# Kernel optimization log

Measured on AMD Instinct MI355X. Metric: run time of the kernel, lower is better.

Reference implementation:

```python
import jax, jax.numpy as jnp
import numpy as np

ROPE_BASE = 10000.0

def apply_rope(x, offset=0):
    # x: [B, H, L, Dh], traditional (interleaved-pair) RoPE
    B, H, L, Dh = x.shape
    pos = jnp.arange(L, dtype=jnp.float32) + offset            # [L]
    freqs = ROPE_BASE ** (-jnp.arange(0, Dh, 2, dtype=jnp.float32) / Dh)  # [Dh/2]
    theta = pos[:, None] * freqs[None, :]                      # [L, Dh/2]
    cos, sin = jnp.cos(theta), jnp.sin(theta)
    x1 = x[..., 0::2]                                          # [B,H,L,Dh/2]
    x2 = x[..., 1::2]
    r1 = x1 * cos - x2 * sin
    r2 = x1 * sin + x2 * cos
    return jnp.stack([r1, r2], axis=-1).reshape(B, H, L, Dh)


def setup_inputs() -> dict:
    key = jax.random.key(0)
    ks = jax.random.split(key, 5)
    B, L, D = 2, 2048, 2048
    s = 1.0 / np.sqrt(D)
    x = jax.random.normal(ks[0], (B, L, D), dtype=jnp.float32)
    # additive causal mask (0 on/below diagonal, -1e9 above)
    mask = jnp.where(jnp.tril(jnp.ones((L, L), dtype=bool)), 0.0, -1e9).astype(jnp.float32)
    Wq = jax.random.normal(ks[1], (D, D), dtype=jnp.float32) * s
    Wk = jax.random.normal(ks[2], (D, D), dtype=jnp.float32) * s
    Wv = jax.random.normal(ks[3], (D, D), dtype=jnp.float32) * s
    Wo = jax.random.normal(ks[4], (D, D), dtype=jnp.float32) * s
    return {"x": x, "mask": mask, "Wq": Wq, "Wk": Wk, "Wv": Wv, "Wo": Wo}


def reference(x, mask, Wq, Wk, Wv, Wo):
    num_heads = 16
    B, L, D = x.shape
    Dh = D // num_heads
    q = (x @ Wq.T).reshape(B, L, num_heads, Dh).transpose(0, 2, 1, 3)  # [B,H,L,Dh]
    k = (x @ Wk.T).reshape(B, L, num_heads, Dh).transpose(0, 2, 1, 3)
    v = (x @ Wv.T).reshape(B, L, num_heads, Dh).transpose(0, 2, 1, 3)
    q = apply_rope(q)
    k = apply_rope(k)
    scale = 1.0 / jnp.sqrt(jnp.float32(Dh))
    scores = jnp.einsum('bhqd,bhkd->bhqk', q * scale, k) + mask  # [B,H,L,L]
    probs = jax.nn.softmax(scores, axis=-1)
    vh = jnp.einsum('bhqk,bhkd->bhqd', probs, v)                 # [B,H,L,Dh]
    vh = vh.transpose(0, 2, 1, 3).reshape(B, L, D)
    out = vh @ Wo.T
    return out, k, v
```

## Files before the change

### kernel.cpp

```cpp
#include <hip/hip_runtime.h>

typedef __attribute__((ext_vector_type(4))) float f32x4;
typedef __attribute__((ext_vector_type(8))) __bf16 bf16x8;

__device__ __forceinline__ unsigned short f2b(float f) {
  unsigned int u = __builtin_bit_cast(unsigned int, f);
  u = (u + 0x7fffu + ((u >> 16) & 1u)) >> 16;
  return (unsigned short)u;
}
__device__ __forceinline__ float b2f(unsigned short h) {
  unsigned int u = ((unsigned int)h) << 16;
  return __builtin_bit_cast(float, u);
}
__device__ __forceinline__ void gl_lds16(const void* g, void* l) {
  __builtin_amdgcn_global_load_lds(
      (const __attribute__((address_space(1))) void*)g,
      (__attribute__((address_space(3))) void*)l, 16, 0, 0);
}

__global__ void cast_kernel(const float* __restrict__ src,
                            unsigned short* __restrict__ dst, int n4) {
  int i = blockIdx.x * blockDim.x + threadIdx.x;
  if (i >= n4) return;
  float4 v = ((const float4*)src)[i];
  ushort4 o;
  o.x = f2b(v.x); o.y = f2b(v.y); o.z = f2b(v.z); o.w = f2b(v.w);
  ((ushort4*)dst)[i] = o;
}

__global__ void cast4_kernel(const float* __restrict__ s0, const float* __restrict__ s1,
                             const float* __restrict__ s2, const float* __restrict__ s3,
                             unsigned short* __restrict__ d0, unsigned short* __restrict__ d1,
                             unsigned short* __restrict__ d2, unsigned short* __restrict__ d3,
                             int n4) {
  int i = blockIdx.x * blockDim.x + threadIdx.x;
  if (i >= n4) return;
  const float* src = blockIdx.y == 0 ? s0 : blockIdx.y == 1 ? s1 : blockIdx.y == 2 ? s2 : s3;
  unsigned short* dst = blockIdx.y == 0 ? d0 : blockIdx.y == 1 ? d1 : blockIdx.y == 2 ? d2 : d3;
  float4 v = ((const float4*)src)[i];
  ushort4 o;
  o.x = f2b(v.x); o.y = f2b(v.y); o.z = f2b(v.z); o.w = f2b(v.w);
  ((ushort4*)dst)[i] = o;
}

__global__ void rope_table_kernel(float2* __restrict__ tab) {
  int idx = blockIdx.x * blockDim.x + threadIdx.x;
  int l = idx >> 6, i = idx & 63;
  float freq = powf(10000.0f, -(float)(2 * i) / 128.0f);
  float th = (float)l * freq;
  tab[idx] = make_float2(cosf(th), sinf(th));
}

__global__ void rope_apply_kernel(unsigned short* __restrict__ qb,
                                  unsigned short* __restrict__ kb,
                                  unsigned short* __restrict__ vb,
                                  float* __restrict__ kout,
                                  float* __restrict__ vout,
                                  const float2* __restrict__ tab) {
  const float QS = 0.12751743f;
  int z = blockIdx.y;
  int p = blockIdx.x * blockDim.x + threadIdx.x;
  int i = p & 63;
  int t = p >> 6;
  int h = t & 15; t >>= 4;
  int l = t & 2047;
  int b = t >> 11;
  int base = ((b * 2048 + l) * 2048) + h * 128 + 2 * i;
  int obase = ((b * 16 + h) * 2048 + l) * 128 + 2 * i;
  if (z == 2) {
    vout[obase] = b2f(vb[base]);
    vout[obase + 1] = b2f(vb[base + 1]);
  } else {
    unsigned short* buf = z ? kb : qb;
    float x1 = b2f(buf[base]), x2 = b2f(buf[base + 1]);
    float2 cs = tab[l * 64 + i];
    float r1 = x1 * cs.x - x2 * cs.y;
    float r2 = x1 * cs.y + x2 * cs.x;
    if (z == 1) {
      buf[base] = f2b(r1);
      buf[base + 1] = f2b(r2);
      kout[obase] = r1; kout[obase + 1] = r2;
    } else {
      buf[base] = f2b(r1 * QS);
      buf[base + 1] = f2b(r2 * QS);
    }
  }
}

__global__ __launch_bounds__(256) void transpose_v_kernel(const unsigned short* __restrict__ vb,
                                                          unsigned short* __restrict__ vt) {
  __shared__ unsigned short t[32][33];
  int bz = blockIdx.z;
  int b = bz >> 4, h = bz & 15;
  int l0 = blockIdx.x * 32, d0 = blockIdx.y * 32;
  const unsigned short* src = vb + (size_t)b * 2048 * 2048 + h * 128;
  unsigned short* dst = vt + (size_t)bz * 128 * 2048;
  int tx = threadIdx.x & 31, ty = threadIdx.x >> 5;
#pragma unroll
  for (int i = 0; i < 4; ++i)
    t[ty + 8 * i][tx] = src[(size_t)(l0 + ty + 8 * i) * 2048 + d0 + tx];
  __syncthreads();
#pragma unroll
  for (int i = 0; i < 4; ++i)
    dst[(size_t)(d0 + ty + 8 * i) * 2048 + l0 + tx] = t[tx][ty + 8 * i];
}

template <int BM, int NBN, int OUT_F32>
__global__ __launch_bounds__(512, 2) void gemm4(const unsigned short* __restrict__ A,
                                                const unsigned short* __restrict__ W,
                                                void* __restrict__ C) {
  constexpr int K = 2048, NT = 32;
  constexpr int AH = BM / 2;
  constexpr int MF = BM / 64;
  constexpr int AQ = AH / 64;
  __shared__ unsigned short Asm[2][2][AH * 64];
  __shared__ unsigned short Bsm[2][2][128 * 64];

  const int tid = threadIdx.x, lane = tid & 63, wv = tid >> 6;
  const int wr = wv >> 2, wc = wv & 3;
  const int ln = lane & 15, kg = lane >> 4;

  const int cpx = (int)gridDim.x >> 3;
  const int swzb = ((int)blockIdx.x & 7) * cpx + ((int)blockIdx.x >> 3);
  const int bm = swzb / NBN, bn = swzb % NBN;
  const int m0 = bm * BM, n0 = bn * 256;

  const int rr = lane >> 3;
  const int sws = ((lane & 7) ^ (rr & 7)) * 8;
  const unsigned short* pA = A + (size_t)(m0 + wv * 8 * AQ + rr) * K + sws;
  const unsigned short* pB = W + (size_t)(n0 + wv * 16 + rr) * K + sws;

#define STA_(dd, hh, tt)                                                         \
  { _Pragma("unroll") for (int q = 0; q < AQ; ++q)                               \
      gl_lds16(pA + ((size_t)(hh)*AH + q * 8) * K + (size_t)(tt)*64,             \
               &Asm[dd][hh][(wv * 8 * AQ + q * 8) * 64 + lane * 8]); }
#define STB_(dd, hh, tt)                                                         \
  { _Pragma("unroll") for (int q = 0; q < 2; ++q)                                \
      gl_lds16(pB + ((size_t)(hh)*128 + q * 8) * K + (size_t)(tt)*64,            \
               &Bsm[dd][hh][(wv * 16 + q * 8) * 64 + lane * 8]); }

  const int sw0 = (kg ^ (ln & 7)) * 8;
  const int sw1 = ((4 + kg) ^ (ln & 7)) * 8;
  const int rae = (wr * (AH / 2) + ln) * 64;
  const int rbe = (wc * 32 + ln) * 64;

  f32x4 acc[2 * MF][4] = {};
  bf16x8 aA[MF][2], bB[2][2][2];

#define LDA_(dd, mh)                                                              \
  { _Pragma("unroll") for (int mf = 0; mf < MF; ++mf) {                           \
      aA[mf][0] = *(const bf16x8*)&Asm[dd][mh][rae + mf * 1024 + sw0];            \
      aA[mf][1] = *(const bf16x8*)&Asm[dd][mh][rae + mf * 1024 + sw1];            \
    } }
#define LDB_(dd, bh)                                                              \
  { _Pragma("unroll") for (int nf = 0; nf < 2; ++nf) {                            \
      bB[bh][nf][0] = *(const bf16x8*)&Bsm[dd][bh][rbe + nf * 1024 + sw0];        \
      bB[bh][nf][1] = *(const bf16x8*)&Bsm[dd][bh][rbe + nf * 1024 + sw1];        \
    } }

#define QMM(mh, bh)                                                               \
  {                                                                               \
    __builtin_amdgcn_s_setprio(1);                                                \
    _Pragma("unroll") for (int mf = 0; mf < MF; ++mf)                             \
        _Pragma("unroll") for (int nf = 0; nf < 2; ++nf) {                        \
      acc[(mh)*MF + mf][(bh)*2 + nf] = __builtin_amdgcn_mfma_f32_16x16x32_bf16(   \
          aA[mf][0], bB[bh][nf][0], acc[(mh)*MF + mf][(bh)*2 + nf], 0, 0, 0);     \
      acc[(mh)*MF + mf][(bh)*2 + nf] = __builtin_amdgcn_mfma_f32_16x16x32_bf16(   \
          aA[mf][1], bB[bh][nf][1], acc[(mh)*MF + mf][(bh)*2 + nf], 0, 0, 0);     \
    }                                                                             \
    __builtin_amdgcn_s_setprio(0);                                                \
  }

#define BAR   { __builtin_amdgcn_s_barrier(); __builtin_amdgcn_sched_barrier(0); }
#define VWAIT                                                                     \
  { if (BM == 256) { asm volatile("s_waitcnt vmcnt(4)" ::: "memory"); }           \
    else { asm volatile("s_waitcnt vmcnt(3)" ::: "memory"); } }
#define VW0   { asm volatile("s_waitcnt vmcnt(0)" ::: "memory"); }

  STA_(0, 0, 0); STB_(0, 0, 0); STB_(0, 1, 0); STA_(0, 1, 0);
  STA_(1, 0, 1); STB_(1, 1, 1);
  VWAIT;

  for (int T = 0; T < NT; T += 2) {
    const bool more = (T + 2) < NT;
    LDA_(0, 0); LDB_(0, 0);
    STB_(1, 0, T + 1);
    BAR; QMM(0, 0); BAR;
    LDB_(0, 1);
    STA_(1, 1, T + 1);
    BAR; QMM(0, 1); BAR;
    LDA_(0, 1);
    if (more) STA_(0, 0, T + 2);
    BAR; QMM(1, 1); BAR;
    if (more) { STB_(0, 1, T + 2); VWAIT; } else { VW0; }
    BAR; QMM(1, 0); BAR;
    LDA_(1, 0); LDB_(1, 0);
    if (more) STB_(0, 0, T + 2);
    BAR; QMM(0, 0); BAR;
    LDB_(1, 1);
    if (more) STA_(0, 1, T + 2);
    BAR; QMM(0, 1); BAR;
    LDA_(1, 1);
    if (more) STA_(1, 0, T + 3);
    BAR; QMM(1, 1); BAR;
    if (more) { STB_(1, 1, T + 3); VWAIT; }
    BAR; QMM(1, 0); BAR;
  }

  const int mat = bn >> 3;
  unsigned short* Cb = (unsigned short*)C;
  float* Cf = (float*)C;
#pragma unroll
  for (int mh = 0; mh < 2; ++mh)
#pragma unroll
    for (int mf = 0; mf < MF; ++mf)
#pragma unroll
      for (int j = 0; j < 4; ++j) {
        int row = m0 + mh * AH + wr * (AH / 2) + mf * 16 + kg * 4 + j;
        size_t rb = (size_t)mat * 8388608 + (size_t)row * 2048 + (size_t)((bn & 7) * 256);
#pragma unroll
        for (int bh = 0; bh < 2; ++bh)
#pragma unroll
          for (int nf = 0; nf < 2; ++nf) {
            int col = bh * 128 + wc * 32 + nf * 16 + ln;
            float v = acc[mh * MF + mf][bh * 2 + nf][j];
            if (OUT_F32) Cf[rb + col] = v;
            else Cb[rb + col] = f2b(v);
          }
      }
#undef STA_
#undef STB_
#undef LDA_
#undef LDB_
#undef QMM
#undef BAR
#undef VWAIT
#undef VW0
}

__global__ __launch_bounds__(256, 2) void attn3_kernel(const unsigned short* __restrict__ Qb,
                                                       const unsigned short* __restrict__ Kb,
                                                       const unsigned short* __restrict__ Vt,
                                                       unsigned short* __restrict__ Ob) {
  __shared__ unsigned short KS[2][8192];
  __shared__ unsigned short VS[2][8192];
  __shared__ unsigned short PS[4][2048];
  const int D = 2048, L = 2048;
  int tid = threadIdx.x, lane = tid & 63, w = tid >> 6;
  int ln = lane & 15, kg = lane >> 4;
  int bid = blockIdx.x;
  int g = bid >> 5, bh = bid & 31;
  int qt = (g < 8) ? (15 - g) : (g - 8);
  int b = bh >> 4, h = bh & 15;
  const size_t base = (size_t)b * L * D + h * 128;
  const unsigned short* Kp = Kb + base;
  const unsigned short* Qp = Qb + base;
  unsigned short* Op = Ob + base;
  const unsigned short* Vp = Vt + (size_t)bh * 128 * L;

  int q0 = qt * 128;
  int qw0 = q0 + w * 32;

  bf16x8 aq[2][4];
#pragma unroll
  for (int m = 0; m < 2; ++m)
#pragma unroll
    for (int kc = 0; kc < 4; ++kc)
      aq[m][kc] = *(const bf16x8*)&Qp[(size_t)(qw0 + m * 16 + ln) * D + kc * 32 + kg * 8];

  f32x4 o[2][8] = {};
  float m2[2][4], ls[2][4];
#pragma unroll
  for (int m = 0; m < 2; ++m)
#pragma unroll
    for (int j = 0; j < 4; ++j) { m2[m][j] = -1e30f; ls[m][j] = 0.f; }

  int l16 = lane >> 4, l8 = lane >> 3, l7 = lane & 7;

#define STAGE(T, NB)                                                                   \
  {                                                                                    \
    int kv0_ = (T) << 6;                                                               \
    _Pragma("unroll") for (int i = 0; i < 4; ++i) {                                    \
      int cK = w * 4 + i;                                                              \
      int r = cK * 4 + l16;                                                            \
      int sw = ln ^ (r & 7);                                                           \
      gl_lds16(Kp + (size_t)(kv0_ + r) * D + sw * 8, &KS[NB][cK * 512 + lane * 8]);    \
      int dh = cK * 8 + l8;                                                            \
      int sv = l7 ^ (dh & 7);                                                          \
      gl_lds16(Vp + (size_t)dh * L + kv0_ + sv * 8, &VS[NB][cK * 512 + lane * 8]);     \
    }                                                                                  \
  }

  int nt = 2 * qt + 2;
  int mask_t = 2 * qt + (w >> 1);

  STAGE(0, 0);
  __syncthreads();

  for (int t = 0; t < nt; ++t) {
    int cur = t & 1;
    if (t + 1 < nt) STAGE(t + 1, cur ^ 1);

    if (t <= mask_t) {
      int kv0 = t << 6;
      f32x4 s[2][4] = {};
#pragma unroll
      for (int n = 0; n < 4; ++n)
#pragma unroll
        for (int kc = 0; kc < 4; ++kc) {
          bf16x8 bk = *(const bf16x8*)&KS[cur][(n * 16 + ln) * 128 + (((kc << 2) + kg) ^ (ln & 7)) * 8];
          s[0][n] = __builtin_amdgcn_mfma_f32_16x16x32_bf16(aq[0][kc], bk, s[0][n], 0, 0, 0);
          s[1][n] = __builtin_amdgcn_mfma_f32_16x16x32_bf16(aq[1][kc], bk, s[1][n], 0, 0, 0);
        }
      if (t == mask_t) {
#pragma unroll
        for (int m = 0; m < 2; ++m)
#pragma unroll
          for (int n = 0; n < 4; ++n)
#pragma unroll
            for (int j = 0; j < 4; ++j)
              if (kv0 + n * 16 + ln > qw0 + m * 16 + kg * 4 + j) s[m][n][j] = -1e30f;
      }
      float pmax[2][4];
      bool near = true;
#pragma unroll
      for (int m = 0; m < 2; ++m)
#pragma unroll
        for (int j = 0; j < 4; ++j) {
          pmax[m][j] = fmaxf(fmaxf(s[m][0][j], s[m][1][j]), fmaxf(s[m][2][j], s[m][3][j]));
          near = near && (pmax[m][j] <= m2[m][j] + 8.0f);
        }
      if (!__all(near)) {
#pragma unroll
        for (int m = 0; m < 2; ++m)
#pragma unroll
          for (int j = 0; j < 4; ++j) {
            float mx = pmax[m][j];
#pragma unroll
            for (int d = 1; d < 16; d <<= 1) mx = fmaxf(mx, __shfl_xor(mx, d));
            mx = fmaxf(mx, m2[m][j]);
            float al = __builtin_amdgcn_exp2f(m2[m][j] - mx);
            m2[m][j] = mx;
            ls[m][j] *= al;
#pragma unroll
            for (int dt = 0; dt < 8; ++dt) o[m][dt][j] *= al;
          }
      }
#pragma unroll
      for (int m = 0; m < 2; ++m)
#pragma unroll
        for (int j = 0; j < 4; ++j) {
          int row = m * 16 + kg * 4 + j;
          float acc = 0.f;
#pragma unroll
          for (int n = 0; n < 4; ++n) {
            float p = __builtin_amdgcn_exp2f(s[m][n][j] - m2[m][j]);
            acc += p;
            unsigned int u = __builtin_bit_cast(unsigned int, p);
            PS[w][row * 64 + (((n * 2 + (ln >> 3)) ^ (row & 7)) * 8) + (ln & 7)] =
                (unsigned short)(u >> 16);
          }
          ls[m][j] += acc;
        }
#pragma unroll
      for (int kst = 0; kst < 2; ++kst) {
        bf16x8 ap0 = *(const bf16x8*)&PS[w][(ln) * 64 + (((kst << 2) + kg) ^ (ln & 7)) * 8];
        bf16x8 ap1 = *(const bf16x8*)&PS[w][(16 + ln) * 64 + (((kst << 2) + kg) ^ (ln & 7)) * 8];
#pragma unroll
        for (int dt = 0; dt < 8; ++dt) {
          bf16x8 bv = *(const bf16x8*)&VS[cur][(dt * 16 + ln) * 64 + (((kst << 2) + kg) ^ (ln & 7)) * 8];
          o[0][dt] = __builtin_amdgcn_mfma_f32_16x16x32_bf16(ap0, bv, o[0][dt], 0, 0, 0);
          o[1][dt] = __builtin_amdgcn_mfma_f32_16x16x32_bf16(ap1, bv, o[1][dt], 0, 0, 0);
        }
      }
    }
    __syncthreads();
  }
#undef STAGE

#pragma unroll
  for (int m = 0; m < 2; ++m)
#pragma unroll
    for (int j = 0; j < 4; ++j) {
      float tsum = ls[m][j];
#pragma unroll
      for (int d = 1; d < 16; d <<= 1) tsum += __shfl_xor(tsum, d);
      float inv = 1.0f / tsum;
      int row = qw0 + m * 16 + kg * 4 + j;
#pragma unroll
      for (int dt = 0; dt < 8; ++dt)
        Op[(size_t)row * D + dt * 16 + ln] = f2b(o[m][dt][j] * inv);
    }
}

extern "C" void kernel_launch(void* const* d_in, const int* in_sizes, int n_in,
                              void* d_out, int out_size, void* d_ws, size_t ws_size,
                              hipStream_t stream) {
  const float* x  = (const float*)d_in[0];
  const float* Wq = (const float*)d_in[2];
  const float* Wk = (const float*)d_in[3];
  const float* Wv = (const float*)d_in[4];
  const float* Wo = (const float*)d_in[5];

  char* ws = (char*)d_ws;
  unsigned short* xb  = (unsigned short*)(ws + 0);
  unsigned short* wqb = (unsigned short*)(ws + 16777216);
  unsigned short* wkb = (unsigned short*)(ws + 25165824);
  unsigned short* wvb = (unsigned short*)(ws + 33554432);
  unsigned short* wob = (unsigned short*)(ws + 41943040);
  unsigned short* qb  = (unsigned short*)(ws + 50331648);
  unsigned short* kb  = (unsigned short*)(ws + 67108864);
  unsigned short* vb  = (unsigned short*)(ws + 83886080);
  float2* tab         = (float2*)(ws + 100663296);
  unsigned short* vt  = wqb;
  unsigned short* ob  = xb;

  float* out  = (float*)d_out;
  float* kout = out + 8388608;
  float* vout = out + 16777216;

  cast_kernel<<<8192, 256, 0, stream>>>(x, xb, 2097152);
  cast4_kernel<<<dim3(4096, 4), 256, 0, stream>>>(Wq, Wk, Wv, Wo, wqb, wkb, wvb, wob, 1048576);
  rope_table_kernel<<<512, 256, 0, stream>>>(tab);

  gemm4<256, 24, 0><<<384, 512, 0, stream>>>(xb, wqb, qb);

  transpose_v_kernel<<<dim3(64, 4, 32), 256, 0, stream>>>(vb, vt);

  rope_apply_kernel<<<dim3(16384, 3), 256, 0, stream>>>(qb, kb, vb, kout, vout, tab);

  attn3_kernel<<<512, 256, 0, stream>>>(qb, kb, vt, ob);

  gemm4<128, 8, 1><<<256, 512, 0, stream>>>(ob, wob, out);
}
```

Baseline: 306.6 us.

## Fuse RoPE into QKV GEMM epilogue and V output into transpose

Removes the standalone rope_apply kernel. RoPE rotation, Q scaling and the fp32 K output are now computed in the QKV GEMM epilogue, with the pair partner fetched by a lane shuffle. The fp32 V output is written from the V transpose kernel. This avoids re-reading and re-writing the q/k/v bf16 buffers and one launch, at the cost of a heavier epilogue with table loads and scattered kout writes. It also swaps the order of the LDA/LDB fragment loads in the main loop.

```diff
diff --git a/kernel.cpp b/kernel.cpp
--- a/kernel.cpp
+++ b/kernel.cpp
@@ -51,44 +51,9 @@
   tab[idx] = make_float2(cosf(th), sinf(th));
 }
 
-__global__ void rope_apply_kernel(unsigned short* __restrict__ qb,
-                                  unsigned short* __restrict__ kb,
-                                  unsigned short* __restrict__ vb,
-                                  float* __restrict__ kout,
-                                  float* __restrict__ vout,
-                                  const float2* __restrict__ tab) {
-  const float QS = 0.12751743f;
-  int z = blockIdx.y;
-  int p = blockIdx.x * blockDim.x + threadIdx.x;
-  int i = p & 63;
-  int t = p >> 6;
-  int h = t & 15; t >>= 4;
-  int l = t & 2047;
-  int b = t >> 11;
-  int base = ((b * 2048 + l) * 2048) + h * 128 + 2 * i;
-  int obase = ((b * 16 + h) * 2048 + l) * 128 + 2 * i;
-  if (z == 2) {
-    vout[obase] = b2f(vb[base]);
-    vout[obase + 1] = b2f(vb[base + 1]);
-  } else {
-    unsigned short* buf = z ? kb : qb;
-    float x1 = b2f(buf[base]), x2 = b2f(buf[base + 1]);
-    float2 cs = tab[l * 64 + i];
-    float r1 = x1 * cs.x - x2 * cs.y;
-    float r2 = x1 * cs.y + x2 * cs.x;
-    if (z == 1) {
-      buf[base] = f2b(r1);
-      buf[base + 1] = f2b(r2);
-      kout[obase] = r1; kout[obase + 1] = r2;
-    } else {
-      buf[base] = f2b(r1 * QS);
-      buf[base + 1] = f2b(r2 * QS);
-    }
-  }
-}
-
 __global__ __launch_bounds__(256) void transpose_v_kernel(const unsigned short* __restrict__ vb,
-                                                          unsigned short* __restrict__ vt) {
+                                                          unsigned short* __restrict__ vt,
+                                                          float* __restrict__ vout) {
   __shared__ unsigned short t[32][33];
   int bz = blockIdx.z;
   int b = bz >> 4, h = bz & 15;
@@ -97,18 +62,23 @@
   unsigned short* dst = vt + (size_t)bz * 128 * 2048;
   int tx = threadIdx.x & 31, ty = threadIdx.x >> 5;
 #pragma unroll
-  for (int i = 0; i < 4; ++i)
-    t[ty + 8 * i][tx] = src[(size_t)(l0 + ty + 8 * i) * 2048 + d0 + tx];
+  for (int i = 0; i < 4; ++i) {
+    unsigned short u = src[(size_t)(l0 + ty + 8 * i) * 2048 + d0 + tx];
+    t[ty + 8 * i][tx] = u;
+    vout[((size_t)bz * 2048 + l0 + ty + 8 * i) * 128 + d0 + tx] = b2f(u);
+  }
   __syncthreads();
 #pragma unroll
   for (int i = 0; i < 4; ++i)
     dst[(size_t)(d0 + ty + 8 * i) * 2048 + l0 + tx] = t[tx][ty + 8 * i];
 }
 
-template <int BM, int NBN, int OUT_F32>
-__global__ __launch_bounds__(512, 2) void gemm4(const unsigned short* __restrict__ A,
+template <int BM, int NBN, int EPI>
+__global__ __launch_bounds__(512, 2) void gemm5(const unsigned short* __restrict__ A,
                                                 const unsigned short* __restrict__ W,
-                                                void* __restrict__ C) {
+                                                void* __restrict__ C,
+                                                float* __restrict__ kout,
+                                                const float2* __restrict__ tab) {
   constexpr int K = 2048, NT = 32;
   constexpr int AH = BM / 2;
   constexpr int MF = BM / 64;
@@ -183,7 +153,7 @@
 
   for (int T = 0; T < NT; T += 2) {
     const bool more = (T + 2) < NT;
-    LDA_(0, 0); LDB_(0, 0);
+    LDB_(0, 0); LDA_(0, 0);
     STB_(1, 0, T + 1);
     BAR; QMM(0, 0); BAR;
     LDB_(0, 1);
@@ -194,7 +164,7 @@
     BAR; QMM(1, 1); BAR;
     if (more) { STB_(0, 1, T + 2); VWAIT; } else { VW0; }
     BAR; QMM(1, 0); BAR;
-    LDA_(1, 0); LDB_(1, 0);
+    LDB_(1, 0); LDA_(1, 0);
     if (more) STB_(0, 0, T + 2);
     BAR; QMM(0, 0); BAR;
     LDB_(1, 1);
@@ -210,6 +180,7 @@
   const int mat = bn >> 3;
   unsigned short* Cb = (unsigned short*)C;
   float* Cf = (float*)C;
+  const float QS = 0.12751743f;
 #pragma unroll
   for (int mh = 0; mh < 2; ++mh)
 #pragma unroll
@@ -218,14 +189,34 @@
       for (int j = 0; j < 4; ++j) {
         int row = m0 + mh * AH + wr * (AH / 2) + mf * 16 + kg * 4 + j;
         size_t rb = (size_t)mat * 8388608 + (size_t)row * 2048 + (size_t)((bn & 7) * 256);
+        int l = row & 2047, b = row >> 11;
 #pragma unroll
         for (int bh = 0; bh < 2; ++bh)
 #pragma unroll
           for (int nf = 0; nf < 2; ++nf) {
             int col = bh * 128 + wc * 32 + nf * 16 + ln;
             float v = acc[mh * MF + mf][bh * 2 + nf][j];
-            if (OUT_F32) Cf[rb + col] = v;
-            else Cb[rb + col] = f2b(v);
+            if (EPI == 2) {
+              Cf[rb + col] = v;
+            } else {
+              float res;
+              if (mat == 2) {
+                res = v;
+              } else {
+                int cc = (bn & 7) * 256 + col;
+                int dh = cc & 127;
+                float p = __shfl_xor(v, 1);
+                float2 cs = tab[l * 64 + (dh >> 1)];
+                res = (ln & 1) ? fmaf(p, cs.y, v * cs.x) : fmaf(v, cs.x, -(p * cs.y));
+                if (mat == 0) {
+                  res *= QS;
+                } else {
+                  int h = cc >> 7;
+                  kout[((size_t)(b * 16 + h) * 2048 + l) * 128 + dh] = res;
+                }
+              }
+              Cb[rb + col] = f2b(res);
+            }
           }
       }
 #undef STA_
@@ -423,13 +414,11 @@
   cast4_kernel<<<dim3(4096, 4), 256, 0, stream>>>(Wq, Wk, Wv, Wo, wqb, wkb, wvb, wob, 1048576);
   rope_table_kernel<<<512, 256, 0, stream>>>(tab);
 
-  gemm4<256, 24, 0><<<384, 512, 0, stream>>>(xb, wqb, qb);
-
-  transpose_v_kernel<<<dim3(64, 4, 32), 256, 0, stream>>>(vb, vt);
-
-  rope_apply_kernel<<<dim3(16384, 3), 256, 0, stream>>>(qb, kb, vb, kout, vout, tab);
+  gemm5<256, 24, 1><<<384, 512, 0, stream>>>(xb, wqb, qb, kout, tab);
+
+  transpose_v_kernel<<<dim3(64, 4, 32), 256, 0, stream>>>(vb, vt, vout);
 
   attn3_kernel<<<512, 256, 0, stream>>>(qb, kb, vt, ob);
 
-  gemm4<128, 8, 1><<<256, 512, 0, stream>>>(ob, wob, out);
-}
+  gemm5<128, 8, 2><<<256, 512, 0, stream>>>(ob, wob, out, nullptr, nullptr);
+}
```

Result: no change. 310.0 us (+1.1%).
